# Optimization experiments

Measured on AMD Instinct MI355X. Metric: run time of the kernel, lower is better.

## Reference

```python
import jax, jax.numpy as jnp
import numpy as np

B, T, N, D = 8, 192, 64, 512
H = 8
DH = D // H
C = 8


def setup_inputs() -> dict:
    key = jax.random.key(0)
    ks = jax.random.split(key, 10)
    s = 1.0 / np.sqrt(D)
    return {
        "x": jax.random.normal(ks[0], (B, T, N, D), dtype=jnp.float32),
        "Wq_w": jax.random.normal(ks[1], (D, D), dtype=jnp.float32) * s,
        "Wq_b": jnp.zeros((D,), dtype=jnp.float32),
        "Wv_w": jax.random.normal(ks[2], (D, D), dtype=jnp.float32) * s,
        "Wv_b": jnp.zeros((D,), dtype=jnp.float32),
        "Wk": jax.random.normal(ks[3], (C, D, D), dtype=jnp.float32) * s,
        "bk": jnp.zeros((C, D), dtype=jnp.float32),
        "proj_w": jax.random.normal(ks[4], (D, D), dtype=jnp.float32) * s,
        "proj_b": jnp.zeros((D,), dtype=jnp.float32),
        "cluster_ids": jax.random.randint(ks[5], (N,), 0, C, dtype=jnp.int64),
    }


def reference(x, Wq_w, Wq_b, Wv_w, Wv_b, Wk, bk, proj_w, proj_b, cluster_ids):
    # torch Linear: y = x @ W.T + b
    Q = jnp.einsum('btnd,ed->btne', x, Wq_w) + Wq_b
    V = jnp.einsum('btnd,ed->btne', x, Wv_w) + Wv_b
    # per-cluster K projection == per-node weight gather (grouped GEMM)
    Wk_n = Wk[cluster_ids]          # [N, D, D]
    bk_n = bk[cluster_ids]          # [N, D]
    K = jnp.einsum('btnd,nde->btne', x, Wk_n) + bk_n

    def split_heads(z):
        # [B,T,N,D] -> [B,N,H,T,DH]
        return z.reshape(B, T, N, H, DH).transpose(0, 2, 3, 1, 4)

    Qh, Kh, Vh = split_heads(Q), split_heads(K), split_heads(V)
    scores = jnp.einsum('bnhtd,bnhsd->bnhts', Qh, Kh) / np.sqrt(DH).astype(np.float32)
    attn = jax.nn.softmax(scores, axis=-1)
    out_h = jnp.einsum('bnhts,bnhsd->bnhtd', attn, Vh)
    out = out_h.transpose(0, 3, 1, 2, 4).reshape(B, T, N, D)
    return jnp.einsum('btnd,ed->btne', out, proj_w) + proj_b
```

## Files before the change

kernel.cpp:

```cpp
#include <hip/hip_runtime.h>
#include <hip/hip_bf16.h>

typedef __bf16 bf16x8 __attribute__((ext_vector_type(8)));
typedef float  f32x4  __attribute__((ext_vector_type(4)));

#define MFMA16(a, b, c) __builtin_amdgcn_mfma_f32_16x16x32_bf16(a, b, c, 0, 0, 0)

__device__ __forceinline__ void async16(const __bf16* g, __bf16* l) {
    __builtin_amdgcn_global_load_lds(
        (const __attribute__((address_space(1))) unsigned int*)g,
        (__attribute__((address_space(3))) unsigned int*)l, 16, 0, 0);
}


__global__ void k_cast3(const float* __restrict__ wq, const float* __restrict__ wv,
                        const float* __restrict__ wp,
                        __bf16* __restrict__ oq, __bf16* __restrict__ ov,
                        __bf16* __restrict__ op) {
    int i = blockIdx.x * 256 + threadIdx.x;
    oq[i] = (__bf16)wq[i];
    ov[i] = (__bf16)wv[i];
    op[i] = (__bf16)wp[i];
}

__global__ void k_twk(const float* __restrict__ wk, __bf16* __restrict__ o) {
    int i = blockIdx.x * 256 + threadIdx.x;
    int c = i >> 18;
    int r = i & 262143;
    int d = r >> 9;
    int e = r & 511;
    o[(c << 18) + (e << 9) + d] = (__bf16)wk[i];
}

__global__ void k_castx(const float* __restrict__ x, __bf16* __restrict__ o) {
    size_t i = ((size_t)blockIdx.x * 256 + threadIdx.x) * 8;
    float4 f0 = *(const float4*)(x + i);
    float4 f1 = *(const float4*)(x + i + 4);
    bf16x8 v;
    v[0] = (__bf16)f0.x; v[1] = (__bf16)f0.y; v[2] = (__bf16)f0.z; v[3] = (__bf16)f0.w;
    v[4] = (__bf16)f1.x; v[5] = (__bf16)f1.y; v[6] = (__bf16)f1.z; v[7] = (__bf16)f1.w;
    *(bf16x8*)(o + i) = v;
}

__launch_bounds__(512, 2)
__global__ void k_qkv(const __bf16* __restrict__ xb,
                      const __bf16* __restrict__ WqE, const __bf16* __restrict__ WvE,
                      const __bf16* __restrict__ WkE,
                      const float* __restrict__ bq, const float* __restrict__ bv,
                      const float* __restrict__ bk, const int* __restrict__ cid,
                      __bf16* __restrict__ Qw, __bf16* __restrict__ Kw,
                      __bf16* __restrict__ Vw) {
    const int g   = blockIdx.y * 36 + blockIdx.x;
    const int s   = (g & 7) * 288 + (g >> 3);
    const int n   = s / 36;
    const int r36 = s - n * 36;
    const int mx  = r36 / 6;
    const int ey  = r36 - mx * 6;
    const int m0  = mx * 256;
    const int e0  = ey * 256;
    const int seg  = e0 >> 9;
    const int eoff = e0 & 511;
    const int c    = cid[n];

    const __bf16* Wb = (seg == 0) ? WqE : (seg == 1) ? WvE : (WkE + ((size_t)c << 18));
    __bf16*       Ob = (seg == 0) ? Qw : (seg == 1) ? Vw : Kw;

    __shared__ __align__(16) __bf16 Ar[4][256 * 32];
    __shared__ __align__(16) __bf16 Br[4][256 * 32];

    const int tid  = threadIdx.x;
    const int lane = tid & 63;
    const int w    = tid >> 6;
    const int wm2  = w >> 2;
    const int wn4  = w & 3;
    const int l15  = lane & 15, qd = lane >> 4;

    const int sr  = tid >> 2;
    const int sp  = tid & 3;
    const int sch = (sp ^ (sr & 3)) * 8;
    const __bf16* aG0 = xb + ((size_t)(m0 + sr) * 64 + n) * 512 + sch;
    const __bf16* aG1 = aG0 + (size_t)128 * 64 * 512;
    const __bf16* bG0 = Wb + ((size_t)(eoff + sr) << 9) + sch;
    const __bf16* bG1 = bG0 + ((size_t)128 << 9);

    const int cro   = (qd ^ (l15 & 3)) * 8;
    const int arow0 = (wm2 * 128 + l15) * 32;
    const int brow0 = (wn4 * 64 + l15) * 32;

    f32x4 acc[8][4];
#pragma unroll
    for (int i = 0; i < 8; ++i)
#pragma unroll
        for (int j = 0; j < 4; ++j) acc[i][j] = (f32x4){0.f, 0.f, 0.f, 0.f};

    auto issue = [&](int t) {
        const int slot = t & 3;
        const int k0 = t * 32;
        __bf16* ad = &Ar[slot][tid * 8];
        __bf16* bd = &Br[slot][tid * 8];
        async16(aG0 + k0, ad);
        async16(aG1 + k0, ad + 4096);
        async16(bG0 + k0, bd);
        async16(bG1 + k0, bd + 4096);
    };
    auto compute = [&](int slot) {
        const __bf16* Asl = Ar[slot];
        const __bf16* Bsl = Br[slot];
        bf16x8 bfr[4], af[8];
#pragma unroll
        for (int j = 0; j < 4; ++j)
            bfr[j] = *(const bf16x8*)&Bsl[brow0 + j * 512 + cro];
#pragma unroll
        for (int i = 0; i < 8; ++i)
            af[i] = *(const bf16x8*)&Asl[arow0 + i * 512 + cro];
        asm volatile("s_waitcnt lgkmcnt(0)" ::: "memory");
        __builtin_amdgcn_sched_barrier(0);
        __builtin_amdgcn_s_setprio(1);
#pragma unroll
        for (int i = 0; i < 8; ++i)
#pragma unroll
            for (int j = 0; j < 4; ++j)
                acc[i][j] = MFMA16(af[i], bfr[j], acc[i][j]);
        __builtin_amdgcn_s_setprio(0);
    };

    issue(0); issue(1); issue(2);
    asm volatile("s_waitcnt vmcnt(8)" ::: "memory");
    __builtin_amdgcn_s_barrier();
    __builtin_amdgcn_sched_barrier(0);

    for (int t = 0; t < 13; ++t) {
        issue(t + 3);
        compute(t & 3);
        asm volatile("s_waitcnt vmcnt(8)" ::: "memory");
        __builtin_amdgcn_s_barrier();
        __builtin_amdgcn_sched_barrier(0);
    }
    compute(1);
    asm volatile("s_waitcnt vmcnt(4)" ::: "memory");
    __builtin_amdgcn_s_barrier();
    __builtin_amdgcn_sched_barrier(0);
    compute(2);
    asm volatile("s_waitcnt vmcnt(0)" ::: "memory");
    __builtin_amdgcn_s_barrier();
    __builtin_amdgcn_sched_barrier(0);
    compute(3);

    float bias[4];
#pragma unroll
    for (int j = 0; j < 4; ++j) {
        int e = eoff + wn4 * 64 + j * 16 + l15;
        bias[j] = (seg == 0) ? bq[e] : (seg == 1) ? bv[e] : bk[(c << 9) + e];
    }
#pragma unroll
    for (int i = 0; i < 8; ++i) {
#pragma unroll
        for (int rx = 0; rx < 4; ++rx) {
            int m  = m0 + wm2 * 128 + i * 16 + qd * 4 + rx;
            int bb = m / 192;
            int tt = m - bb * 192;
            size_t ro = ((size_t)(bb * 64 + n) * 192 + tt) << 9;
#pragma unroll
            for (int j = 0; j < 4; ++j) {
                int e = eoff + wn4 * 64 + j * 16 + l15;
                Ob[ro + e] = (__bf16)(acc[i][j][rx] + bias[j]);
            }
        }
    }
}

__launch_bounds__(768)
__global__ void k_attn(const __bf16* __restrict__ Qw, const __bf16* __restrict__ Kw,
                       const __bf16* __restrict__ Vw, __bf16* __restrict__ Ow) {
    const int h = blockIdx.x, n = blockIdx.y, b = blockIdx.z;
    __shared__ __align__(16) __bf16 Ks[192 * 72];
    __shared__ __align__(16) __bf16 Vt[64 * 192];
    __shared__ __align__(16) __bf16 Ps[192 * 200];

    const int tid  = threadIdx.x;
    const int lane = tid & 63, w = tid >> 6;
    const int l15  = lane & 15, qd = lane >> 4;
    const size_t base = ((size_t)((b * 64 + n) * 192) << 9) + h * 64;

    for (int i = tid; i < 1536; i += 768) {
        int row = i >> 3, pp = i & 7;
        *(bf16x8*)&Ks[row * 72 + 8 * pp] =
            *(const bf16x8*)(Kw + base + ((size_t)row << 9) + 8 * pp);
    }
#pragma unroll
    for (int rr = 0; rr < 2; ++rr) {
        int idx = rr * 768 + tid;
        int e = idx & 63, sb = idx >> 6;
        bf16x8 v;
#pragma unroll
        for (int j = 0; j < 8; ++j)
            v[j] = Vw[base + (size_t)(sb * 8 + j) * 512 + e];
        *(bf16x8*)&Vt[e * 192 + ((sb ^ (e & 7)) * 8)] = v;
    }
    __syncthreads();

    const __bf16* qp = Qw + base + ((size_t)(16 * w + l15) << 9) + 8 * qd;
    bf16x8 aq0 = *(const bf16x8*)(qp);
    bf16x8 aq1 = *(const bf16x8*)(qp + 32);

    f32x4 S[12];
#pragma unroll
    for (int ct = 0; ct < 12; ++ct) {
        f32x4 acc = (f32x4){0.f, 0.f, 0.f, 0.f};
        bf16x8 b0 = *(const bf16x8*)&Ks[(16 * ct + l15) * 72 + 8 * qd];
        bf16x8 b1 = *(const bf16x8*)&Ks[(16 * ct + l15) * 72 + 32 + 8 * qd];
        acc = MFMA16(aq0, b0, acc);
        acc = MFMA16(aq1, b1, acc);
        S[ct] = acc;
    }

    float mx[4] = {-1e30f, -1e30f, -1e30f, -1e30f};
#pragma unroll
    for (int ct = 0; ct < 12; ++ct)
#pragma unroll
        for (int rx = 0; rx < 4; ++rx) mx[rx] = fmaxf(mx[rx], S[ct][rx]);
#pragma unroll
    for (int mk = 1; mk < 16; mk <<= 1)
#pragma unroll
        for (int rx = 0; rx < 4; ++rx) mx[rx] = fmaxf(mx[rx], __shfl_xor(mx[rx], mk, 64));

    const float sc = 0.125f * 1.44269504088896f;
    float sm[4] = {0.f, 0.f, 0.f, 0.f};
#pragma unroll
    for (int ct = 0; ct < 12; ++ct) {
#pragma unroll
        for (int rx = 0; rx < 4; ++rx) {
            float pe = exp2f((S[ct][rx] - mx[rx]) * sc);
            sm[rx] += pe;
            Ps[(w * 16 + qd * 4 + rx) * 200 + 16 * ct + l15] = (__bf16)pe;
        }
    }
#pragma unroll
    for (int mk = 1; mk < 16; mk <<= 1)
#pragma unroll
        for (int rx = 0; rx < 4; ++rx) sm[rx] += __shfl_xor(sm[rx], mk, 64);

    __syncthreads();

    float inv[4];
#pragma unroll
    for (int rx = 0; rx < 4; ++rx) inv[rx] = 1.f / sm[rx];

#pragma unroll
    for (int et = 0; et < 4; ++et) {
        f32x4 acc = (f32x4){0.f, 0.f, 0.f, 0.f};
#pragma unroll
        for (int sn = 0; sn < 6; ++sn) {
            bf16x8 pa = *(const bf16x8*)&Ps[(w * 16 + l15) * 200 + sn * 32 + 8 * qd];
            bf16x8 vb = *(const bf16x8*)
                &Vt[(et * 16 + l15) * 192 + (((sn * 4 + qd) ^ (l15 & 7)) * 8)];
            acc = MFMA16(pa, vb, acc);
        }
#pragma unroll
        for (int rx = 0; rx < 4; ++rx) {
            int t = 16 * w + 4 * qd + rx;
            Ow[base + ((size_t)t << 9) + et * 16 + l15] = (__bf16)(acc[rx] * inv[rx]);
        }
    }
}

__launch_bounds__(256)
__global__ void k_proj(const __bf16* __restrict__ Ow, const __bf16* __restrict__ WpE,
                       const float* __restrict__ bp, float* __restrict__ out) {
    const int n  = blockIdx.z;
    const int m0 = blockIdx.x * 128;
    const int e0 = blockIdx.y * 128;
    __shared__ __align__(16) __bf16 As[128 * 64];
    __shared__ __align__(16) __bf16 Bs[128 * 64];

    const int tid  = threadIdx.x;
    const int lane = tid & 63, w = tid >> 6;
    const int wm   = w >> 1, wn = w & 1;
    const int l15  = lane & 15, qd = lane >> 4;
    const int lr   = lane >> 3, lc = lane & 7;
    const int sc8  = (lc ^ lr) * 8;
    const int sw   = l15 & 7;

    const __bf16* agj[4];
#pragma unroll
    for (int j = 0; j < 4; ++j) {
        int m  = m0 + w * 32 + j * 8 + lr;
        int bb = m / 192;
        int tt = m - bb * 192;
        agj[j] = Ow + (((size_t)(bb * 64 + n) * 192 + tt) << 9) + sc8;
    }
    __bf16* al = As + w * 2048 + lr * 64 + lc * 8;
    const __bf16* bg  = WpE + ((size_t)(e0 + w * 32 + lr) << 9) + sc8;
    __bf16*       blp = Bs + w * 2048 + lr * 64 + lc * 8;

    f32x4 acc[4][4];
#pragma unroll
    for (int i = 0; i < 4; ++i)
#pragma unroll
        for (int j = 0; j < 4; ++j) acc[i][j] = (f32x4){0.f, 0.f, 0.f, 0.f};

    for (int kk = 0; kk < 8; ++kk) {
        const int k0 = kk * 64;
        __syncthreads();
#pragma unroll
        for (int j = 0; j < 4; ++j) {
            async16(agj[j] + k0, al + j * 512);
            async16(bg + j * 4096 + k0, blp + j * 512);
        }
        __syncthreads();

#pragma unroll
        for (int kc = 0; kc < 2; ++kc) {
            const int co = ((kc * 4 + qd) ^ sw) * 8;
            bf16x8 a0 = *(const bf16x8*)&As[(wm * 64 + l15) * 64 + co];
            bf16x8 a1 = *(const bf16x8*)&As[(wm * 64 + 16 + l15) * 64 + co];
            bf16x8 a2 = *(const bf16x8*)&As[(wm * 64 + 32 + l15) * 64 + co];
            bf16x8 a3 = *(const bf16x8*)&As[(wm * 64 + 48 + l15) * 64 + co];
#pragma unroll
            for (int j = 0; j < 4; ++j) {
                bf16x8 fb = *(const bf16x8*)&Bs[(wn * 64 + j * 16 + l15) * 64 + co];
                acc[0][j] = MFMA16(a0, fb, acc[0][j]);
                acc[1][j] = MFMA16(a1, fb, acc[1][j]);
                acc[2][j] = MFMA16(a2, fb, acc[2][j]);
                acc[3][j] = MFMA16(a3, fb, acc[3][j]);
            }
        }
    }

    float bias[4];
#pragma unroll
    for (int j = 0; j < 4; ++j) bias[j] = bp[e0 + wn * 64 + j * 16 + l15];
#pragma unroll
    for (int i = 0; i < 4; ++i) {
#pragma unroll
        for (int rx = 0; rx < 4; ++rx) {
            int m = m0 + wm * 64 + i * 16 + qd * 4 + rx;
            size_t ro = ((size_t)(m * 64 + n)) << 9;
#pragma unroll
            for (int j = 0; j < 4; ++j) {
                int e = e0 + wn * 64 + j * 16 + l15;
                out[ro + e] = acc[i][j][rx] + bias[j];
            }
        }
    }
}

extern "C" void kernel_launch(void* const* d_in, const int* in_sizes, int n_in,
                              void* d_out, int out_size, void* d_ws, size_t ws_size,
                              hipStream_t stream) {
    const float* x    = (const float*)d_in[0];
    const float* Wq_w = (const float*)d_in[1];
    const float* Wq_b = (const float*)d_in[2];
    const float* Wv_w = (const float*)d_in[3];
    const float* Wv_b = (const float*)d_in[4];
    const float* Wk   = (const float*)d_in[5];
    const float* bk   = (const float*)d_in[6];
    const float* Wp   = (const float*)d_in[7];
    const float* bp   = (const float*)d_in[8];
    const int*   cid  = (const int*)d_in[9];
    float* out = (float*)d_out;

    __bf16* WqE = (__bf16*)d_ws;
    __bf16* WvE = WqE + (1 << 18);
    __bf16* WpE = WvE + (1 << 18);
    __bf16* WkE = WpE + (1 << 18);
    __bf16* Qw  = WkE + (8 << 18);
    __bf16* Kw  = Qw + 50331648LL;
    __bf16* Vw  = Kw + 50331648LL;
    __bf16* XO  = Vw + 50331648LL;

    k_cast3<<<1024, 256, 0, stream>>>(Wq_w, Wv_w, Wp, WqE, WvE, WpE);
    k_twk<<<8192, 256, 0, stream>>>(Wk, WkE);
    k_castx<<<24576, 256, 0, stream>>>(x, XO);
    k_qkv<<<dim3(36, 64), 512, 0, stream>>>(XO, WqE, WvE, WkE, Wq_b, Wv_b, bk, cid,
                                            Qw, Kw, Vw);
    k_attn<<<dim3(8, 64, 8), 768, 0, stream>>>(Qw, Kw, Vw, XO);
    k_proj<<<dim3(12, 4, 64), 256, 0, stream>>>(XO, WpE, bp, out);
}
```

Baseline: 802.2 us.

## Retile projection GEMM into pipelined 256x256 kernel and retune QKV swizzle

```diff
diff --git a/kernel.cpp b/kernel.cpp
--- a/kernel.cpp
+++ b/kernel.cpp
@@ -77,13 +77,13 @@
 
     const int sr  = tid >> 2;
     const int sp  = tid & 3;
-    const int sch = (sp ^ (sr & 3)) * 8;
+    const int sch = (sp ^ ((sr >> 1) & 3)) * 8;
     const __bf16* aG0 = xb + ((size_t)(m0 + sr) * 64 + n) * 512 + sch;
     const __bf16* aG1 = aG0 + (size_t)128 * 64 * 512;
     const __bf16* bG0 = Wb + ((size_t)(eoff + sr) << 9) + sch;
     const __bf16* bG1 = bG0 + ((size_t)128 << 9);
 
-    const int cro   = (qd ^ (l15 & 3)) * 8;
+    const int cro   = (qd ^ ((l15 >> 1) & 3)) * 8;
     const int arow0 = (wm2 * 128 + l15) * 32;
     const int brow0 = (wn4 * 64 + l15) * 32;
 
@@ -113,8 +113,6 @@
 #pragma unroll
         for (int i = 0; i < 8; ++i)
             af[i] = *(const bf16x8*)&Asl[arow0 + i * 512 + cro];
-        asm volatile("s_waitcnt lgkmcnt(0)" ::: "memory");
-        __builtin_amdgcn_sched_barrier(0);
         __builtin_amdgcn_s_setprio(1);
 #pragma unroll
         for (int i = 0; i < 8; ++i)
@@ -127,23 +125,19 @@
     issue(0); issue(1); issue(2);
     asm volatile("s_waitcnt vmcnt(8)" ::: "memory");
     __builtin_amdgcn_s_barrier();
-    __builtin_amdgcn_sched_barrier(0);
 
     for (int t = 0; t < 13; ++t) {
         issue(t + 3);
         compute(t & 3);
         asm volatile("s_waitcnt vmcnt(8)" ::: "memory");
         __builtin_amdgcn_s_barrier();
-        __builtin_amdgcn_sched_barrier(0);
     }
     compute(1);
     asm volatile("s_waitcnt vmcnt(4)" ::: "memory");
     __builtin_amdgcn_s_barrier();
-    __builtin_amdgcn_sched_barrier(0);
     compute(2);
     asm volatile("s_waitcnt vmcnt(0)" ::: "memory");
     __builtin_amdgcn_s_barrier();
-    __builtin_amdgcn_sched_barrier(0);
     compute(3);
 
     float bias[4];
@@ -264,81 +258,107 @@
     }
 }
 
-__launch_bounds__(256)
+__launch_bounds__(512, 2)
 __global__ void k_proj(const __bf16* __restrict__ Ow, const __bf16* __restrict__ WpE,
                        const float* __restrict__ bp, float* __restrict__ out) {
-    const int n  = blockIdx.z;
-    const int m0 = blockIdx.x * 128;
-    const int e0 = blockIdx.y * 128;
-    __shared__ __align__(16) __bf16 As[128 * 64];
-    __shared__ __align__(16) __bf16 Bs[128 * 64];
+    const int g   = blockIdx.x;
+    const int s   = (g & 7) * 96 + (g >> 3);
+    const int n   = s / 12;
+    const int r12 = s - n * 12;
+    const int mx  = r12 >> 1;
+    const int ey  = r12 & 1;
+    const int m0  = mx * 256;
+    const int e0  = ey * 256;
+
+    __shared__ __align__(16) __bf16 Ar[4][256 * 32];
+    __shared__ __align__(16) __bf16 Br[4][256 * 32];
 
     const int tid  = threadIdx.x;
-    const int lane = tid & 63, w = tid >> 6;
-    const int wm   = w >> 1, wn = w & 1;
+    const int lane = tid & 63;
+    const int w    = tid >> 6;
+    const int wm2  = w >> 2;
+    const int wn4  = w & 3;
     const int l15  = lane & 15, qd = lane >> 4;
-    const int lr   = lane >> 3, lc = lane & 7;
-    const int sc8  = (lc ^ lr) * 8;
-    const int sw   = l15 & 7;
-
-    const __bf16* agj[4];
-#pragma unroll
-    for (int j = 0; j < 4; ++j) {
-        int m  = m0 + w * 32 + j * 8 + lr;
-        int bb = m / 192;
-        int tt = m - bb * 192;
-        agj[j] = Ow + (((size_t)(bb * 64 + n) * 192 + tt) << 9) + sc8;
-    }
-    __bf16* al = As + w * 2048 + lr * 64 + lc * 8;
-    const __bf16* bg  = WpE + ((size_t)(e0 + w * 32 + lr) << 9) + sc8;
-    __bf16*       blp = Bs + w * 2048 + lr * 64 + lc * 8;
-
-    f32x4 acc[4][4];
-#pragma unroll
-    for (int i = 0; i < 4; ++i)
+
+    const int sr  = tid >> 2;
+    const int sp  = tid & 3;
+    const int sch = (sp ^ ((sr >> 1) & 3)) * 8;
+    int mA0 = m0 + sr;       int bb0 = mA0 / 192, tt0 = mA0 - bb0 * 192;
+    int mA1 = m0 + 128 + sr; int bb1 = mA1 / 192, tt1 = mA1 - bb1 * 192;
+    const __bf16* aG0 = Ow + (((size_t)(bb0 * 64 + n) * 192 + tt0) << 9) + sch;
+    const __bf16* aG1 = Ow + (((size_t)(bb1 * 64 + n) * 192 + tt1) << 9) + sch;
+    const __bf16* bG0 = WpE + ((size_t)(e0 + sr) << 9) + sch;
+    const __bf16* bG1 = bG0 + ((size_t)128 << 9);
+
+    const int cro   = (qd ^ ((l15 >> 1) & 3)) * 8;
+    const int arow0 = (wm2 * 128 + l15) * 32;
+    const int brow0 = (wn4 * 64 + l15) * 32;
+
+    f32x4 acc[8][4];
+#pragma unroll
+    for (int i = 0; i < 8; ++i)
 #pragma unroll
         for (int j = 0; j < 4; ++j) acc[i][j] = (f32x4){0.f, 0.f, 0.f, 0.f};
 
-    for (int kk = 0; kk < 8; ++kk) {
-        const int k0 = kk * 64;
-        __syncthreads();
-#pragma unroll
-        for (int j = 0; j < 4; ++j) {
-            async16(agj[j] + k0, al + j * 512);
-            async16(bg + j * 4096 + k0, blp + j * 512);
-        }
-        __syncthreads();
-
-#pragma unroll
-        for (int kc = 0; kc < 2; ++kc) {
-            const int co = ((kc * 4 + qd) ^ sw) * 8;
-            bf16x8 a0 = *(const bf16x8*)&As[(wm * 64 + l15) * 64 + co];
-            bf16x8 a1 = *(const bf16x8*)&As[(wm * 64 + 16 + l15) * 64 + co];
-            bf16x8 a2 = *(const bf16x8*)&As[(wm * 64 + 32 + l15) * 64 + co];
-            bf16x8 a3 = *(const bf16x8*)&As[(wm * 64 + 48 + l15) * 64 + co];
+    auto issue = [&](int t) {
+        const int slot = t & 3;
+        const int k0 = t * 32;
+        __bf16* ad = &Ar[slot][tid * 8];
+        __bf16* bd = &Br[slot][tid * 8];
+        async16(aG0 + k0, ad);
+        async16(aG1 + k0, ad + 4096);
+        async16(bG0 + k0, bd);
+        async16(bG1 + k0, bd + 4096);
+    };
+    auto compute = [&](int slot) {
+        const __bf16* Asl = Ar[slot];
+        const __bf16* Bsl = Br[slot];
+        bf16x8 bfr[4], af[8];
+#pragma unroll
+        for (int j = 0; j < 4; ++j)
+            bfr[j] = *(const bf16x8*)&Bsl[brow0 + j * 512 + cro];
+#pragma unroll
+        for (int i = 0; i < 8; ++i)
+            af[i] = *(const bf16x8*)&Asl[arow0 + i * 512 + cro];
+        __builtin_amdgcn_s_setprio(1);
+#pragma unroll
+        for (int i = 0; i < 8; ++i)
+#pragma unroll
+            for (int j = 0; j < 4; ++j)
+                acc[i][j] = MFMA16(af[i], bfr[j], acc[i][j]);
+        __builtin_amdgcn_s_setprio(0);
+    };
+
+    issue(0); issue(1); issue(2);
+    asm volatile("s_waitcnt vmcnt(8)" ::: "memory");
+    __builtin_amdgcn_s_barrier();
+
+    for (int t = 0; t < 13; ++t) {
+        issue(t + 3);
+        compute(t & 3);
+        asm volatile("s_waitcnt vmcnt(8)" ::: "memory");
+        __builtin_amdgcn_s_barrier();
+    }
+    compute(1);
+    asm volatile("s_waitcnt vmcnt(4)" ::: "memory");
+    __builtin_amdgcn_s_barrier();
+    compute(2);
+    asm volatile("s_waitcnt vmcnt(0)" ::: "memory");
+    __builtin_amdgcn_s_barrier();
+    compute(3);
+
+    float bias[4];
+#pragma unroll
+    for (int j = 0; j < 4; ++j) bias[j] = bp[e0 + wn4 * 64 + j * 16 + l15];
+#pragma unroll
+    for (int i = 0; i < 8; ++i) {
+#pragma unroll
+        for (int rx = 0; rx < 4; ++rx) {
+            int m = m0 + wm2 * 128 + i * 16 + qd * 4 + rx;
+            size_t ro = ((size_t)(m * 64 + n)) << 9;
 #pragma unroll
             for (int j = 0; j < 4; ++j) {
-                bf16x8 fb = *(const bf16x8*)&Bs[(wn * 64 + j * 16 + l15) * 64 + co];
-                acc[0][j] = MFMA16(a0, fb, acc[0][j]);
-                acc[1][j] = MFMA16(a1, fb, acc[1][j]);
-                acc[2][j] = MFMA16(a2, fb, acc[2][j]);
-                acc[3][j] = MFMA16(a3, fb, acc[3][j]);
-            }
-        }
-    }
-
-    float bias[4];
-#pragma unroll
-    for (int j = 0; j < 4; ++j) bias[j] = bp[e0 + wn * 64 + j * 16 + l15];
-#pragma unroll
-    for (int i = 0; i < 4; ++i) {
-#pragma unroll
-        for (int rx = 0; rx < 4; ++rx) {
-            int m = m0 + wm * 64 + i * 16 + qd * 4 + rx;
-            size_t ro = ((size_t)(m * 64 + n)) << 9;
-#pragma unroll
-            for (int j = 0; j < 4; ++j) {
-                int e = e0 + wn * 64 + j * 16 + l15;
+                int e = e0 + wn4 * 64 + j * 16 + l15;
                 out[ro + e] = acc[i][j][rx] + bias[j];
             }
         }
@@ -375,5 +395,5 @@
     k_qkv<<<dim3(36, 64), 512, 0, stream>>>(XO, WqE, WvE, WkE, Wq_b, Wv_b, bk, cid,
                                             Qw, Kw, Vw);
     k_attn<<<dim3(8, 64, 8), 768, 0, stream>>>(Qw, Kw, Vw, XO);
-    k_proj<<<dim3(12, 4, 64), 256, 0, stream>>>(XO, WpE, bp, out);
-}
+    k_proj<<<768, 512, 0, stream>>>(XO, WpE, bp, out);
+}
```

Measured after the change: 783.6 us. 2.3% less time.
